# Kernel tuning notes

Hardware: AMD Instinct MI355X
Metric: run time of the kernel (lower is better)

The kernel has to match this reference:

```python
import jax, jax.numpy as jnp
import numpy as np

B, N_IN, N_OUT, DEG = 128, 16384, 8192, 64
N_EDGES = N_OUT * DEG


def setup_inputs() -> dict:
    key = jax.random.key(0)
    k_x, k_src, k_dst, k_w = jax.random.split(key, 4)
    x = jax.random.normal(k_x, (B, N_IN), dtype=jnp.float32)
    # Ragged connectivity flattened to a CSR-like edge list:
    # edge_src[e] -> input feature index, edge_dst[e] -> output unit index.
    edge_src = jax.random.randint(k_src, (N_EDGES,), 0, N_IN, dtype=jnp.int64)
    edge_dst = jnp.sort(jax.random.randint(k_dst, (N_EDGES,), 0, N_OUT, dtype=jnp.int64))
    w = jax.random.normal(k_w, (N_EDGES,), dtype=jnp.float32) * 0.05  # one weight per edge
    bias = jnp.zeros((N_OUT,), dtype=jnp.float32)
    return {"x": x, "w": w, "bias": bias, "edge_src": edge_src, "edge_dst": edge_dst}


def reference(x, w, bias, edge_src, edge_dst):
    # Equivalent to: for each output j, y[:, j] = relu(x[:, edges_j] @ w_j + bias[j])
    # Vectorized as a single gather + weighted scatter-add over the flat edge list.
    n_out = bias.shape[0]
    gathered = x[:, edge_src] * w  # [B, E]
    y = jnp.zeros((x.shape[0], n_out), dtype=x.dtype).at[:, edge_dst].add(gathered)
    return jax.nn.relu(y + bias)
```

## Files before the change

### kernel.cpp

```cpp
#include <hip/hip_runtime.h>

#define B_DIM   128
#define N_IN    16384
#define N_OUT   8192
#define N_EDGES (N_OUT * 64)

#define WAVES_PB 8
#define J_BLK    WAVES_PB
#define THREADS  (WAVES_PB * 64)

__device__ __forceinline__ int lower_bound_dev(const int* __restrict__ a, int n, int v) {
    int lo = 0, hi = n;
    while (lo < hi) {
        int mid = (lo + hi) >> 1;
        if (a[mid] < v) lo = mid + 1; else hi = mid;
    }
    return lo;
}

__global__ void build_rowptr_kernel(const int* __restrict__ dst, int* __restrict__ rp) {
    const int e = blockIdx.x * blockDim.x + threadIdx.x;
    if (e >= N_EDGES) return;
    const int d     = dst[e];
    const int dprev = (e == 0) ? -1 : dst[e - 1];
    for (int j = dprev + 1; j <= d; ++j) rp[j] = e;
    if (e == N_EDGES - 1)
        for (int j = d + 1; j <= N_OUT; ++j) rp[j] = N_EDGES;
}

__global__ __launch_bounds__(256) void transpose_kernel(const float* __restrict__ x,
                                                        float* __restrict__ xT) {
    __shared__ float tile[32][33];
    const int i0 = blockIdx.x * 32;
    const int b0 = blockIdx.y * 32;
    const int tx = threadIdx.x;
    const int ty = threadIdx.y;
#pragma unroll
    for (int r = 0; r < 32; r += 8)
        tile[ty + r][tx] = x[(size_t)(b0 + ty + r) * N_IN + (i0 + tx)];
    __syncthreads();
#pragma unroll
    for (int r = 0; r < 32; r += 8)
        xT[(size_t)(i0 + ty + r) * B_DIM + (b0 + tx)] = tile[tx][ty + r];
}

__global__ __launch_bounds__(THREADS, 8) void sparse_layer_fast(
        const float* __restrict__ xT, const float* __restrict__ w,
        const float* __restrict__ bias, const int* __restrict__ src,
        const int* __restrict__ rp, float* __restrict__ y) {
    __shared__ float tile[J_BLK][132];

    const int tid  = threadIdx.x;
    const int wid  = tid >> 6;
    const int lane = tid & 63;
    const int half = lane >> 5;
    const int bcol = (lane & 31) << 2;
    const int j0   = blockIdx.x * J_BLK;
    const int j    = j0 + wid;

    const int e0 = __builtin_amdgcn_readfirstlane(rp[j]);
    const int e1 = __builtin_amdgcn_readfirstlane(rp[j + 1]);

    float4 acc = {0.f, 0.f, 0.f, 0.f};
    const float4* xrow = (const float4*)xT + (bcol >> 2);

    int e = e0;
    for (; e + 8 <= e1; e += 8) {
#pragma unroll
        for (int p = 0; p < 4; ++p) {
            const int   ea = e + 2 * p;
            const int   sa = src[ea];
            const int   sb = src[ea + 1];
            const float wa = w[ea];
            const float wb = w[ea + 1];
            const int   s  = half ? sb : sa;
            const float wt = half ? wb : wa;
            const float4 v = xrow[(size_t)s * (B_DIM / 4)];
            acc.x = fmaf(v.x, wt, acc.x);
            acc.y = fmaf(v.y, wt, acc.y);
            acc.z = fmaf(v.z, wt, acc.z);
            acc.w = fmaf(v.w, wt, acc.w);
        }
    }
    for (; e < e1; e += 2) {
        const int   sa    = src[e];
        const float wa    = w[e];
        const bool  has_b = (e + 1) < e1;
        const int   sb    = has_b ? src[e + 1] : sa;
        const float wb    = has_b ? w[e + 1] : 0.f;
        const int   s     = half ? sb : sa;
        const float wt    = half ? wb : wa;
        const float4 v = xrow[(size_t)s * (B_DIM / 4)];
        acc.x = fmaf(v.x, wt, acc.x);
        acc.y = fmaf(v.y, wt, acc.y);
        acc.z = fmaf(v.z, wt, acc.z);
        acc.w = fmaf(v.w, wt, acc.w);
    }

    acc.x += __shfl_xor(acc.x, 32, 64);
    acc.y += __shfl_xor(acc.y, 32, 64);
    acc.z += __shfl_xor(acc.z, 32, 64);
    acc.w += __shfl_xor(acc.w, 32, 64);

    if (half == 0) {
        *(float4*)&tile[wid][bcol] = acc;
    }
    __syncthreads();

#pragma unroll
    for (int i = tid; i < B_DIM * J_BLK; i += THREADS) {
        const int bb = i >> 3;
        const int jj = i & (J_BLK - 1);
        const float v = tile[jj][bb] + bias[j0 + jj];
        y[(size_t)bb * N_OUT + (j0 + jj)] = fmaxf(v, 0.f);
    }
}

__global__ __launch_bounds__(THREADS) void sparse_layer_fallback(
        const float* __restrict__ x, const float* __restrict__ w,
        const float* __restrict__ bias, const int* __restrict__ src,
        const int* __restrict__ dst, float* __restrict__ y) {
    __shared__ float tile[J_BLK][130];
    __shared__ int   srp[J_BLK + 1];

    const int tid  = threadIdx.x;
    const int wid  = tid >> 6;
    const int lane = tid & 63;
    const int j0   = blockIdx.x * J_BLK;

    if (tid <= J_BLK) srp[tid] = lower_bound_dev(dst, N_EDGES, j0 + tid);
    __syncthreads();

    const int e0 = srp[wid], e1 = srp[wid + 1];
    const int b0 = lane * 2;
    float acc0 = 0.f, acc1 = 0.f;
    for (int e = e0; e < e1; ++e) {
        const int   s  = src[e];
        const float wt = w[e];
        acc0 = fmaf(x[(size_t)b0 * N_IN + s], wt, acc0);
        acc1 = fmaf(x[(size_t)(b0 + 1) * N_IN + s], wt, acc1);
    }
    tile[wid][b0]     = acc0;
    tile[wid][b0 + 1] = acc1;
    __syncthreads();
#pragma unroll
    for (int i = tid; i < B_DIM * J_BLK; i += THREADS) {
        const int bb = i >> 3;
        const int jj = i & (J_BLK - 1);
        const float v = tile[jj][bb] + bias[j0 + jj];
        y[(size_t)bb * N_OUT + (j0 + jj)] = fmaxf(v, 0.f);
    }
}

extern "C" void kernel_launch(void* const* d_in, const int* in_sizes, int n_in,
                              void* d_out, int out_size, void* d_ws, size_t ws_size,
                              hipStream_t stream) {
    const float* x    = (const float*)d_in[0];
    const float* w    = (const float*)d_in[1];
    const float* bias = (const float*)d_in[2];
    const int*   esrc = (const int*)d_in[3];
    const int*   edst = (const int*)d_in[4];
    float*       y    = (float*)d_out;

    const size_t RP_BYTES = (size_t)(N_OUT + 1) * sizeof(int);
    const size_t XT_OFF   = 65536;
    const size_t XT_BYTES = (size_t)N_IN * B_DIM * sizeof(float);

    const bool has_ws = ws_size >= XT_OFF + XT_BYTES && ws_size >= RP_BYTES;

    int*   rp = (int*)d_ws;
    float* xT = (float*)((char*)d_ws + XT_OFF);

    if (has_ws) {
        build_rowptr_kernel<<<(N_EDGES + 255) / 256, 256, 0, stream>>>(edst, rp);
        transpose_kernel<<<dim3(N_IN / 32, B_DIM / 32), dim3(32, 8), 0, stream>>>(x, xT);
        sparse_layer_fast<<<dim3(N_OUT / J_BLK), THREADS, 0, stream>>>(xT, w, bias, esrc, rp, y);
    } else {
        sparse_layer_fallback<<<dim3(N_OUT / J_BLK), THREADS, 0, stream>>>(x, w, bias, esrc, edst, y);
    }
}
```

Baseline: 98.81 us.

## Split batch dimension into chunks and process eight edges per wave iteration

The sparse layer kernel now splits the 128-wide batch into four 32-column chunks, one per block group. Each wave covers one output row, with eight lanes per edge and eight edges per iteration, and reduces across the edge slots with cross-lane shuffles. This gives four times as many blocks and more independent gathers in flight per wave, aiming to hide gather latency. In exchange, the edge indices and weights are reloaded once per chunk, each gathered row segment shrinks to 128 bytes, and the shuffle reduction is longer.

```diff
diff --git a/kernel.cpp b/kernel.cpp
--- a/kernel.cpp
+++ b/kernel.cpp
@@ -8,6 +8,10 @@
 #define WAVES_PB 8
 #define J_BLK    WAVES_PB
 #define THREADS  (WAVES_PB * 64)
+
+#define CHUNKB   32
+#define NCHUNK   (B_DIM / CHUNKB)
+#define JGROUPS  (N_OUT / J_BLK)
 
 __device__ __forceinline__ int lower_bound_dev(const int* __restrict__ a, int n, int v) {
     int lo = 0, hi = n;
@@ -44,75 +48,61 @@
         xT[(size_t)(i0 + ty + r) * B_DIM + (b0 + tx)] = tile[tx][ty + r];
 }
 
-__global__ __launch_bounds__(THREADS, 8) void sparse_layer_fast(
+__global__ __launch_bounds__(THREADS, 8) void sparse_layer_chunked(
         const float* __restrict__ xT, const float* __restrict__ w,
         const float* __restrict__ bias, const int* __restrict__ src,
         const int* __restrict__ rp, float* __restrict__ y) {
-    __shared__ float tile[J_BLK][132];
+    __shared__ float tile[J_BLK][36];
 
-    const int tid  = threadIdx.x;
-    const int wid  = tid >> 6;
-    const int lane = tid & 63;
-    const int half = lane >> 5;
-    const int bcol = (lane & 31) << 2;
-    const int j0   = blockIdx.x * J_BLK;
-    const int j    = j0 + wid;
+    const int tid   = threadIdx.x;
+    const int wid   = tid >> 6;
+    const int lane  = tid & 63;
+    const int slot  = lane >> 3;
+    const int bl    = lane & 7;
+    const int chunk = blockIdx.x >> 10;
+    const int jg    = blockIdx.x & (JGROUPS - 1);
+    const int cb    = chunk * CHUNKB;
+    const int j0    = jg * J_BLK;
+    const int j     = j0 + wid;
 
     const int e0 = __builtin_amdgcn_readfirstlane(rp[j]);
     const int e1 = __builtin_amdgcn_readfirstlane(rp[j + 1]);
 
     float4 acc = {0.f, 0.f, 0.f, 0.f};
-    const float4* xrow = (const float4*)xT + (bcol >> 2);
+    const float* xbase = xT + cb + 4 * bl;
 
-    int e = e0;
-    for (; e + 8 <= e1; e += 8) {
-#pragma unroll
-        for (int p = 0; p < 4; ++p) {
-            const int   ea = e + 2 * p;
-            const int   sa = src[ea];
-            const int   sb = src[ea + 1];
-            const float wa = w[ea];
-            const float wb = w[ea + 1];
-            const int   s  = half ? sb : sa;
-            const float wt = half ? wb : wa;
-            const float4 v = xrow[(size_t)s * (B_DIM / 4)];
-            acc.x = fmaf(v.x, wt, acc.x);
-            acc.y = fmaf(v.y, wt, acc.y);
-            acc.z = fmaf(v.z, wt, acc.z);
-            acc.w = fmaf(v.w, wt, acc.w);
-        }
-    }
-    for (; e < e1; e += 2) {
-        const int   sa    = src[e];
-        const float wa    = w[e];
-        const bool  has_b = (e + 1) < e1;
-        const int   sb    = has_b ? src[e + 1] : sa;
-        const float wb    = has_b ? w[e + 1] : 0.f;
-        const int   s     = half ? sb : sa;
-        const float wt    = half ? wb : wa;
-        const float4 v = xrow[(size_t)s * (B_DIM / 4)];
+#pragma unroll 2
+    for (int e = e0; e < e1; e += 8) {
+        const int  ee    = e + slot;
+        const bool valid = ee < e1;
+        const int  ec    = valid ? ee : e0;
+        const int  s     = src[ec];
+        const float wt   = valid ? w[ec] : 0.f;
+        const float4 v   = *(const float4*)(xbase + (size_t)s * B_DIM);
         acc.x = fmaf(v.x, wt, acc.x);
         acc.y = fmaf(v.y, wt, acc.y);
         acc.z = fmaf(v.z, wt, acc.z);
         acc.w = fmaf(v.w, wt, acc.w);
     }
 
-    acc.x += __shfl_xor(acc.x, 32, 64);
-    acc.y += __shfl_xor(acc.y, 32, 64);
-    acc.z += __shfl_xor(acc.z, 32, 64);
-    acc.w += __shfl_xor(acc.w, 32, 64);
+#pragma unroll
+    for (int m = 8; m <= 32; m <<= 1) {
+        acc.x += __shfl_xor(acc.x, m, 64);
+        acc.y += __shfl_xor(acc.y, m, 64);
+        acc.z += __shfl_xor(acc.z, m, 64);
+        acc.w += __shfl_xor(acc.w, m, 64);
+    }
 
-    if (half == 0) {
-        *(float4*)&tile[wid][bcol] = acc;
+    if (slot == 0) {
+        *(float4*)&tile[wid][4 * bl] = acc;
     }
     __syncthreads();
 
-#pragma unroll
-    for (int i = tid; i < B_DIM * J_BLK; i += THREADS) {
-        const int bb = i >> 3;
-        const int jj = i & (J_BLK - 1);
+    if (tid < J_BLK * CHUNKB) {
+        const int jj = tid & (J_BLK - 1);
+        const int bb = tid >> 3;
         const float v = tile[jj][bb] + bias[j0 + jj];
-        y[(size_t)bb * N_OUT + (j0 + jj)] = fmaxf(v, 0.f);
+        y[(size_t)(cb + bb) * N_OUT + (j0 + jj)] = fmaxf(v, 0.f);
     }
 }
 
@@ -174,7 +164,7 @@
     if (has_ws) {
         build_rowptr_kernel<<<(N_EDGES + 255) / 256, 256, 0, stream>>>(edst, rp);
         transpose_kernel<<<dim3(N_IN / 32, B_DIM / 32), dim3(32, 8), 0, stream>>>(x, xT);
-        sparse_layer_fast<<<dim3(N_OUT / J_BLK), THREADS, 0, stream>>>(xT, w, bias, esrc, rp, y);
+        sparse_layer_chunked<<<dim3(JGROUPS * NCHUNK), THREADS, 0, stream>>>(xT, w, bias, esrc, rp, y);
     } else {
         sparse_layer_fallback<<<dim3(N_OUT / J_BLK), THREADS, 0, stream>>>(x, w, bias, esrc, edst, y);
     }
```

New measurement: 100.2 us. Within noise of the previous version (+1.4%).
